# Kernel optimization log

Measured on AMD Instinct MI355X. Metric: run time of the kernel, lower is better.

## Reference

```python
import jax, jax.numpy as jnp
import numpy as np


def setup_inputs() -> dict:
    key = jax.random.key(0)
    ks = jax.random.split(key, 5)
    B, S, D = 2, 2048, 1024
    inv = 1.0 / np.sqrt(D)
    inp = {
        "x": jax.random.normal(ks[0], (B, S, D), jnp.float32),
        "Wq": jax.random.normal(ks[1], (D, D), jnp.float32) * inv,
        "bq": jnp.zeros((D,), jnp.float32),
        "Wk": jax.random.normal(ks[2], (D, D), jnp.float32) * inv,
        "bk": jnp.zeros((D,), jnp.float32),
        "Wv": jax.random.normal(ks[3], (D, D), jnp.float32) * inv,
        "bv": jnp.zeros((D,), jnp.float32),
        "Wo": jax.random.normal(ks[4], (D, D), jnp.float32) * inv,
        "bo": jnp.zeros((D,), jnp.float32),
        "num_heads": 16,
        "window_size": 128,
    }
    return inp


def reference(x, Wq, bq, Wk, bk, Wv, bv, Wo, bo, num_heads, window_size):
    B, S, D = x.shape
    H = num_heads
    hd = D // H
    scale = 1.0 / np.sqrt(hd)

    def split_heads(t):  # [B,S,D] -> [B,H,S,hd]
        return t.reshape(B, S, H, hd).transpose(0, 2, 1, 3)

    q = split_heads(x @ Wq + bq)
    k = split_heads(x @ Wk + bk)
    v = split_heads(x @ Wv + bv)

    # dense scores, then sliding-window + causal mask (faithful to original)
    scores = jnp.einsum('bhqd,bhkd->bhqk', q, k) * scale  # [B,H,S,S]
    i = jnp.arange(S)[:, None]
    j = jnp.arange(S)[None, :]
    # position i attends to j in [i - window_size + 1, i]
    mask = (j <= i) & (j > i - window_size)
    scores = jnp.where(mask, scores, -jnp.inf)
    attn_weights = jax.nn.softmax(scores, axis=-1)  # dropout is identity in eval

    out = jnp.einsum('bhqk,bhkd->bhqd', attn_weights, v)  # [B,H,S,hd]
    out = out.transpose(0, 2, 1, 3).reshape(B, S, D)
    return out @ Wo + bo, attn_weights
```

## Files before the change

### kernel.cpp

```cpp
#include <hip/hip_runtime.h>
#include <cmath>

typedef __attribute__((ext_vector_type(8))) __bf16 v8bf;
typedef __attribute__((ext_vector_type(4))) float  v4f;

#define DEV static __device__ __forceinline__

DEV unsigned short f2bf(float f) {
  unsigned u = __builtin_bit_cast(unsigned, f);
  unsigned r = u + 0x7fffu + ((u >> 16) & 1u);
  return (unsigned short)(r >> 16);
}
DEV float bf2f(unsigned short s) {
  return __builtin_bit_cast(float, ((unsigned)s) << 16);
}
DEV v8bf ld8(const unsigned short* p) { return *(const v8bf*)p; }

DEV void gl16(const unsigned short* g, unsigned short* l) {
  __builtin_amdgcn_global_load_lds(
      (const __attribute__((address_space(1))) unsigned int*)g,
      (__attribute__((address_space(3))) unsigned int*)l, 16, 0, 0);
}

DEV void zero_rows(float* __restrict__ wout, int rbase, int wave, int lane) {
  int r0 = rbase + wave * 4;
  for (int rr = 0; rr < 4; rr++) {
    int row = r0 + rr;
    int i = row & 2047;
    int lo = i - 127;
    float* rowp = wout + (size_t)row * 2048;
#pragma unroll
    for (int it = 0; it < 8; it++) {
      int col = it * 256 + lane * 4;
      bool overlap = (col + 3 >= lo) && (col <= i);
      if (!overlap) {
        v4f z = {0.f, 0.f, 0.f, 0.f};
        __builtin_nontemporal_store(z, (v4f*)(rowp + col));
      } else {
#pragma unroll
        for (int e = 0; e < 4; e++) {
          int j = col + e;
          if (j < lo || j > i) rowp[j] = 0.f;
        }
      }
    }
  }
}

__global__ __launch_bounds__(256) void k_prep(const float* __restrict__ x,
                                              const float* __restrict__ Wq,
                                              const float* __restrict__ Wk,
                                              const float* __restrict__ Wv,
                                              const float* __restrict__ Wo,
                                              const float* __restrict__ bq,
                                              const float* __restrict__ bk,
                                              const float* __restrict__ bv,
                                              unsigned short* __restrict__ xb,
                                              unsigned short* __restrict__ WT,
                                              unsigned short* __restrict__ WoT,
                                              float* __restrict__ bqkv) {
  __shared__ float t[32][33];
  int bx = blockIdx.x, tid = threadIdx.x;
  if (bx < 4096) {
    int i = bx * 256 + tid;
    float4 v = ((const float4*)x)[i];
    unsigned lo = (unsigned)f2bf(v.x) | ((unsigned)f2bf(v.y) << 16);
    unsigned hi = (unsigned)f2bf(v.z) | ((unsigned)f2bf(v.w) << 16);
    ((uint2*)xb)[i] = make_uint2(lo, hi);
  } else if (bx < 8192) {
    int rem = bx - 4096;
    int z = rem >> 10, r2 = rem & 1023;
    const float* src = (z == 0) ? Wq : (z == 1) ? Wk : (z == 2) ? Wv : Wo;
    unsigned short* dst = (z < 3) ? WT + z * 1048576 : WoT;
    int n0 = (r2 & 31) * 32, k0 = (r2 >> 5) * 32;
    int tx = tid & 31, ty = tid >> 5;
    for (int r = ty; r < 32; r += 8)
      t[r][tx] = src[(k0 + r) * 1024 + n0 + tx];
    __syncthreads();
    for (int r = ty; r < 32; r += 8)
      dst[(n0 + r) * 1024 + k0 + tx] = f2bf(t[tx][r]);
  } else {
    int i = (bx - 8192) * 256 + tid;
    float v = (i < 1024) ? bq[i] : (i < 2048 ? bk[i - 1024] : bv[i - 2048]);
    bqkv[i] = v;
  }
}

__global__ __launch_bounds__(256) void k_gemm1(const unsigned short* __restrict__ A,
                                               const unsigned short* __restrict__ Bt,
                                               const float* __restrict__ bias,
                                               unsigned short* __restrict__ QK,
                                               unsigned short* __restrict__ Vtg) {
  constexpr int K = 1024;
  __shared__ __attribute__((aligned(16))) unsigned short As[128 * 32];
  __shared__ __attribute__((aligned(16))) unsigned short Bs[128 * 32];
  int tid = threadIdx.x;
  int wave = tid >> 6, lane = tid & 63;
  int gid = blockIdx.x;
  int n0 = (gid % 24) * 128, m0 = (gid / 24) * 128;
  int wm = (wave >> 1) * 64, wn = (wave & 1) * 64;
  int m = lane & 15, q4 = lane >> 4;
  int arow = tid >> 2, acol = (tid & 3) * 8;
  v4f acc[4][4] = {};
  const unsigned short* ga0 = A + (m0 + arow) * K + acol;
  const unsigned short* ga1 = A + (m0 + 64 + arow) * K + acol;
  const unsigned short* gb0 = Bt + (n0 + arow) * K + acol;
  const unsigned short* gb1 = Bt + (n0 + 64 + arow) * K + acol;
  unsigned short* lA0 = As + wave * 512;
  unsigned short* lA1 = As + 2048 + wave * 512;
  unsigned short* lB0 = Bs + wave * 512;
  unsigned short* lB1 = Bs + 2048 + wave * 512;

  for (int kt = 0; kt < K; kt += 32) {
    gl16(ga0 + kt, lA0);
    gl16(ga1 + kt, lA1);
    gl16(gb0 + kt, lB0);
    gl16(gb1 + kt, lB1);
    __syncthreads();
    v8bf af[4], bfv[4];
#pragma unroll
    for (int mt = 0; mt < 4; mt++) af[mt] = ld8(&As[(wm + mt * 16 + m) * 32 + q4 * 8]);
#pragma unroll
    for (int nt = 0; nt < 4; nt++) bfv[nt] = ld8(&Bs[(wn + nt * 16 + m) * 32 + q4 * 8]);
#pragma unroll
    for (int mt = 0; mt < 4; mt++)
#pragma unroll
      for (int nt = 0; nt < 4; nt++)
        acc[mt][nt] = __builtin_amdgcn_mfma_f32_16x16x32_bf16(af[mt], bfv[nt], acc[mt][nt], 0, 0, 0);
    __syncthreads();
  }
  if (n0 < 2048) {
#pragma unroll
    for (int mt = 0; mt < 4; mt++)
#pragma unroll
      for (int nt = 0; nt < 4; nt++) {
        int col = n0 + wn + nt * 16 + m;
        float bb = bias[col];
#pragma unroll
        for (int r = 0; r < 4; r++) {
          int row = m0 + wm + mt * 16 + q4 * 4 + r;
          QK[row * 2048 + col] = f2bf(acc[mt][nt][r] + bb);
        }
      }
  } else {
    int b = m0 >> 11;
#pragma unroll
    for (int mt = 0; mt < 4; mt++)
#pragma unroll
      for (int nt = 0; nt < 4; nt++) {
        int d = n0 - 2048 + wn + nt * 16 + m;
        int h = d >> 6, dd = d & 63;
        float bb = bias[2048 + d];
        int vrow = (b * 16 + h) * 64 + dd;
        int s0 = (m0 + wm + mt * 16 + q4 * 4) & 2047;
        unsigned short u0 = f2bf(acc[mt][nt][0] + bb);
        unsigned short u1 = f2bf(acc[mt][nt][1] + bb);
        unsigned short u2 = f2bf(acc[mt][nt][2] + bb);
        unsigned short u3 = f2bf(acc[mt][nt][3] + bb);
        unsigned lo = (unsigned)u0 | ((unsigned)u1 << 16);
        unsigned hi = (unsigned)u2 | ((unsigned)u3 << 16);
        *(uint2*)&Vtg[(size_t)vrow * 2048 + s0] = make_uint2(lo, hi);
      }
  }
}

__global__ __launch_bounds__(256) void k_attn(const unsigned short* __restrict__ QK,
                                              const unsigned short* __restrict__ Vtg,
                                              unsigned short* __restrict__ Oatt,
                                              float* __restrict__ wout) {
  constexpr int VTS = 208;
  constexpr int PSS = 168;
  __shared__ __attribute__((aligned(16))) unsigned short Vt[64 * VTS];
  __shared__ __attribute__((aligned(16))) unsigned short Ps[4][16 * PSS];
  int tid = threadIdx.x, wave = tid >> 6, lane = tid & 63;
  int b = blockIdx.z, h = blockIdx.y, i0 = blockIdx.x * 64;
  int kbase = i0 - 128;
  const int ld = 2048;
  const unsigned short* Qg = QK + (size_t)b * 2048 * ld + h * 64;
  const unsigned short* Kg = Qg + 1024;

  const unsigned short* vsrc = Vtg + (size_t)(b * 16 + h) * 64 * 2048;
  for (int idx = tid; idx < 1536; idx += 256) {
    int row = idx / 24, c16 = idx % 24;
    int gcol = kbase + c16 * 8;
    if (gcol < 0) gcol = 0;
    v8bf vv = ld8(vsrc + (size_t)row * 2048 + gcol);
    *(v8bf*)&Vt[row * VTS + c16 * 8] = vv;
  }
  {
    int row = tid >> 2, c4 = (tid & 3) * 4;
    *(uint2*)&Vt[row * VTS + 192 + c4] = make_uint2(0u, 0u);
  }
  for (int c = lane; c < 16 * 24; c += 64)
    Ps[wave][(c / 24) * PSS + 144 + (c % 24)] = 0;
  __syncthreads();

  int qb = i0 + wave * 16;
  int m = lane & 15, q4 = lane >> 4;

  const unsigned short* qrow = Qg + (qb + m) * ld;
  v8bf qa0 = ld8(qrow + q4 * 8);
  v8bf qa1 = ld8(qrow + 32 + q4 * 8);

  v4f sc[9];
#pragma unroll
  for (int n = 0; n < 9; n++) {
    int key = kbase + wave * 16 + n * 16 + m;
    int kg = key < 0 ? 0 : key;
    const unsigned short* krow = Kg + kg * ld;
    v8bf kb0 = ld8(krow + q4 * 8);
    v8bf kb1 = ld8(krow + 32 + q4 * 8);
    v4f z = {0.f, 0.f, 0.f, 0.f};
    z = __builtin_amdgcn_mfma_f32_16x16x32_bf16(qa0, kb0, z, 0, 0, 0);
    z = __builtin_amdgcn_mfma_f32_16x16x32_bf16(qa1, kb1, z, 0, 0, 0);
    sc[n] = z;
  }
  float mx[4] = {-3e38f, -3e38f, -3e38f, -3e38f};
#pragma unroll
  for (int n = 0; n < 9; n++)
#pragma unroll
    for (int r = 0; r < 4; r++) {
      int i = qb + q4 * 4 + r;
      int j = kbase + wave * 16 + n * 16 + m;
      float v = sc[n][r] * 0.125f;
      bool ok = (j >= 0) && (j <= i) && (j > i - 128);
      v = ok ? v : -3e38f;
      sc[n][r] = v;
      mx[r] = fmaxf(mx[r], v);
    }
#pragma unroll
  for (int o = 1; o < 16; o <<= 1)
#pragma unroll
    for (int r = 0; r < 4; r++) mx[r] = fmaxf(mx[r], __shfl_xor(mx[r], o, 64));
  float sum[4] = {0.f, 0.f, 0.f, 0.f};
#pragma unroll
  for (int n = 0; n < 9; n++)
#pragma unroll
    for (int r = 0; r < 4; r++) {
      float p = __expf(sc[n][r] - mx[r]);
      sc[n][r] = p;
      sum[r] += p;
    }
#pragma unroll
  for (int o = 1; o < 16; o <<= 1)
#pragma unroll
    for (int r = 0; r < 4; r++) sum[r] += __shfl_xor(sum[r], o, 64);
  float inv[4];
#pragma unroll
  for (int r = 0; r < 4; r++) inv[r] = 1.0f / sum[r];

#pragma unroll
  for (int n = 0; n < 9; n++)
#pragma unroll
    for (int r = 0; r < 4; r++)
      Ps[wave][(q4 * 4 + r) * PSS + n * 16 + m] = f2bf(sc[n][r] * inv[r]);
  __syncthreads();

  v4f oacc[4] = {};
#pragma unroll
  for (int c = 0; c < 5; c++) {
    v8bf pa = ld8(&Ps[wave][m * PSS + c * 32 + q4 * 8]);
#pragma unroll
    for (int dt = 0; dt < 4; dt++) {
      v8bf vb = ld8(&Vt[(dt * 16 + m) * VTS + wave * 16 + c * 32 + q4 * 8]);
      oacc[dt] = __builtin_amdgcn_mfma_f32_16x16x32_bf16(pa, vb, oacc[dt], 0, 0, 0);
    }
  }
#pragma unroll
  for (int dt = 0; dt < 4; dt++)
#pragma unroll
    for (int r = 0; r < 4; r++)
      Oatt[(b * 2048 + qb + q4 * 4 + r) * 1024 + h * 64 + dt * 16 + m] = f2bf(oacc[dt][r]);

  for (int R = 0; R < 16; R++) {
    int iq = qb + R;
    float* rowp = wout + (size_t)((b * 16 + h) * 2048 + iq) * 2048;
    int lo = iq - 127;
    int t0 = R + 1 + lane * 2;
    float p0 = bf2f(Ps[wave][R * PSS + t0]);
    float p1 = bf2f(Ps[wave][R * PSS + t0 + 1]);
    int j0 = lo + lane * 2;
    if (j0 >= 0) rowp[j0] = p0;
    if (j0 + 1 >= 0) rowp[j0 + 1] = p1;
  }
}

__global__ __launch_bounds__(256) void k_tail(const unsigned short* __restrict__ Oat,
                                              const unsigned short* __restrict__ WoT,
                                              const float* __restrict__ bo,
                                              float* __restrict__ out,
                                              float* __restrict__ wout) {
  __shared__ __attribute__((aligned(16))) unsigned short As[128 * 32];
  __shared__ __attribute__((aligned(16))) unsigned short Bs[128 * 32];
  int tid = threadIdx.x, wave = tid >> 6, lane = tid & 63;
  int bx = blockIdx.x;

  if (bx >= 256) {
    zero_rows(wout, (bx - 256) * 16, wave, lane);
    return;
  }
  constexpr int K = 1024;
  int n0 = (bx & 7) * 128, m0 = (bx >> 3) * 128;
  int wm = (wave >> 1) * 64, wn = (wave & 1) * 64;
  int m = lane & 15, q4 = lane >> 4;
  int arow = tid >> 2, acol = (tid & 3) * 8;
  v4f acc[4][4] = {};
  const unsigned short* ga0 = Oat + (m0 + arow) * K + acol;
  const unsigned short* ga1 = Oat + (m0 + 64 + arow) * K + acol;
  const unsigned short* gb0 = WoT + (n0 + arow) * K + acol;
  const unsigned short* gb1 = WoT + (n0 + 64 + arow) * K + acol;
  unsigned short* lA0 = As + wave * 512;
  unsigned short* lA1 = As + 2048 + wave * 512;
  unsigned short* lB0 = Bs + wave * 512;
  unsigned short* lB1 = Bs + 2048 + wave * 512;
  for (int kt = 0; kt < K; kt += 32) {
    gl16(ga0 + kt, lA0);
    gl16(ga1 + kt, lA1);
    gl16(gb0 + kt, lB0);
    gl16(gb1 + kt, lB1);
    __syncthreads();
    v8bf af[4], bfv[4];
#pragma unroll
    for (int mt = 0; mt < 4; mt++) af[mt] = ld8(&As[(wm + mt * 16 + m) * 32 + q4 * 8]);
#pragma unroll
    for (int nt = 0; nt < 4; nt++) bfv[nt] = ld8(&Bs[(wn + nt * 16 + m) * 32 + q4 * 8]);
#pragma unroll
    for (int mt = 0; mt < 4; mt++)
#pragma unroll
      for (int nt = 0; nt < 4; nt++)
        acc[mt][nt] = __builtin_amdgcn_mfma_f32_16x16x32_bf16(af[mt], bfv[nt], acc[mt][nt], 0, 0, 0);
    __syncthreads();
  }
#pragma unroll
  for (int mt = 0; mt < 4; mt++)
#pragma unroll
    for (int nt = 0; nt < 4; nt++) {
      int col = n0 + wn + nt * 16 + m;
      float bb = bo[col];
#pragma unroll
      for (int r = 0; r < 4; r++) {
        int row = m0 + wm + mt * 16 + q4 * 4 + r;
        out[row * 1024 + col] = acc[mt][nt][r] + bb;
      }
    }
}

extern "C" void kernel_launch(void* const* d_in, const int* in_sizes, int n_in,
                              void* d_out, int out_size, void* d_ws, size_t ws_size,
                              hipStream_t stream) {
  (void)in_sizes; (void)n_in; (void)out_size; (void)ws_size;
  const float* x  = (const float*)d_in[0];
  const float* Wq = (const float*)d_in[1];
  const float* bq = (const float*)d_in[2];
  const float* Wk = (const float*)d_in[3];
  const float* bk = (const float*)d_in[4];
  const float* Wv = (const float*)d_in[5];
  const float* bv = (const float*)d_in[6];
  const float* Wo = (const float*)d_in[7];
  const float* bo = (const float*)d_in[8];

  char* ws = (char*)d_ws;
  unsigned short* xb   = (unsigned short*)(ws);
  unsigned short* WT   = (unsigned short*)(ws + 8388608);
  unsigned short* WoT  = (unsigned short*)(ws + 14680064);
  float*          bqkv = (float*)(ws + 16777216);
  unsigned short* QK   = (unsigned short*)(ws + 16789504);
  unsigned short* Oat  = (unsigned short*)(ws + 33566720);
  unsigned short* Vtg  = (unsigned short*)(ws + 41955328);

  float* out  = (float*)d_out;
  float* wout = out + 4194304;

  k_prep<<<8204, 256, 0, stream>>>(x, Wq, Wk, Wv, Wo, bq, bk, bv, xb, WT, WoT, bqkv);
  k_gemm1<<<768, 256, 0, stream>>>(xb, WT, bqkv, QK, Vtg);
  k_attn<<<dim3(32, 16, 2), 256, 0, stream>>>(QK, Vtg, Oat, wout);
  k_tail<<<4352, 256, 0, stream>>>(Oat, WoT, bo, out, wout);
}
```

Measured before the change: 657.8 us.

## Stage compact band weights and write full attention rows in one streaming pass

The attention kernel now writes each row's 128 banded probabilities as packed bf16 into a compact workspace buffer instead of scattering them into the dense fp32 weight matrix. The tail kernel's zeroing blocks then write every full row once with nontemporal vector stores, filling band entries from that buffer. The old split of masked partial zero writes plus separate scattered band writes is gone. The attention kernel also drops its LDS staging of V and reads V fragments directly from global memory, removing a block barrier at the cost of uncoalesced global loads.

```diff
diff --git a/kernel.cpp b/kernel.cpp
--- a/kernel.cpp
+++ b/kernel.cpp
@@ -20,31 +20,6 @@
   __builtin_amdgcn_global_load_lds(
       (const __attribute__((address_space(1))) unsigned int*)g,
       (__attribute__((address_space(3))) unsigned int*)l, 16, 0, 0);
-}
-
-DEV void zero_rows(float* __restrict__ wout, int rbase, int wave, int lane) {
-  int r0 = rbase + wave * 4;
-  for (int rr = 0; rr < 4; rr++) {
-    int row = r0 + rr;
-    int i = row & 2047;
-    int lo = i - 127;
-    float* rowp = wout + (size_t)row * 2048;
-#pragma unroll
-    for (int it = 0; it < 8; it++) {
-      int col = it * 256 + lane * 4;
-      bool overlap = (col + 3 >= lo) && (col <= i);
-      if (!overlap) {
-        v4f z = {0.f, 0.f, 0.f, 0.f};
-        __builtin_nontemporal_store(z, (v4f*)(rowp + col));
-      } else {
-#pragma unroll
-        for (int e = 0; e < 4; e++) {
-          int j = col + e;
-          if (j < lo || j > i) rowp[j] = 0.f;
-        }
-      }
-    }
-  }
 }
 
 __global__ __launch_bounds__(256) void k_prep(const float* __restrict__ x,
@@ -167,10 +142,8 @@
 __global__ __launch_bounds__(256) void k_attn(const unsigned short* __restrict__ QK,
                                               const unsigned short* __restrict__ Vtg,
                                               unsigned short* __restrict__ Oatt,
-                                              float* __restrict__ wout) {
-  constexpr int VTS = 208;
+                                              unsigned short* __restrict__ cb) {
   constexpr int PSS = 168;
-  __shared__ __attribute__((aligned(16))) unsigned short Vt[64 * VTS];
   __shared__ __attribute__((aligned(16))) unsigned short Ps[4][16 * PSS];
   int tid = threadIdx.x, wave = tid >> 6, lane = tid & 63;
   int b = blockIdx.z, h = blockIdx.y, i0 = blockIdx.x * 64;
@@ -178,22 +151,10 @@
   const int ld = 2048;
   const unsigned short* Qg = QK + (size_t)b * 2048 * ld + h * 64;
   const unsigned short* Kg = Qg + 1024;
-
   const unsigned short* vsrc = Vtg + (size_t)(b * 16 + h) * 64 * 2048;
-  for (int idx = tid; idx < 1536; idx += 256) {
-    int row = idx / 24, c16 = idx % 24;
-    int gcol = kbase + c16 * 8;
-    if (gcol < 0) gcol = 0;
-    v8bf vv = ld8(vsrc + (size_t)row * 2048 + gcol);
-    *(v8bf*)&Vt[row * VTS + c16 * 8] = vv;
-  }
-  {
-    int row = tid >> 2, c4 = (tid & 3) * 4;
-    *(uint2*)&Vt[row * VTS + 192 + c4] = make_uint2(0u, 0u);
-  }
+
   for (int c = lane; c < 16 * 24; c += 64)
     Ps[wave][(c / 24) * PSS + 144 + (c % 24)] = 0;
-  __syncthreads();
 
   int qb = i0 + wave * 16;
   int m = lane & 15, q4 = lane >> 4;
@@ -260,9 +221,12 @@
 #pragma unroll
   for (int c = 0; c < 5; c++) {
     v8bf pa = ld8(&Ps[wave][m * PSS + c * 32 + q4 * 8]);
+    int jc = kbase + wave * 16 + c * 32 + q4 * 8;
+    if (jc < 0) jc = 0;
+    if (jc > 2040) jc = 2040;
 #pragma unroll
     for (int dt = 0; dt < 4; dt++) {
-      v8bf vb = ld8(&Vt[(dt * 16 + m) * VTS + wave * 16 + c * 32 + q4 * 8]);
+      v8bf vb = ld8(vsrc + (size_t)(dt * 16 + m) * 2048 + jc);
       oacc[dt] = __builtin_amdgcn_mfma_f32_16x16x32_bf16(pa, vb, oacc[dt], 0, 0, 0);
     }
   }
@@ -273,15 +237,10 @@
       Oatt[(b * 2048 + qb + q4 * 4 + r) * 1024 + h * 64 + dt * 16 + m] = f2bf(oacc[dt][r]);
 
   for (int R = 0; R < 16; R++) {
-    int iq = qb + R;
-    float* rowp = wout + (size_t)((b * 16 + h) * 2048 + iq) * 2048;
-    int lo = iq - 127;
-    int t0 = R + 1 + lane * 2;
-    float p0 = bf2f(Ps[wave][R * PSS + t0]);
-    float p1 = bf2f(Ps[wave][R * PSS + t0 + 1]);
-    int j0 = lo + lane * 2;
-    if (j0 >= 0) rowp[j0] = p0;
-    if (j0 + 1 >= 0) rowp[j0 + 1] = p1;
+    int row = (b * 16 + h) * 2048 + qb + R;
+    unsigned short p0 = Ps[wave][R * PSS + R + 1 + lane * 2];
+    unsigned short p1 = Ps[wave][R * PSS + R + 2 + lane * 2];
+    ((unsigned*)cb)[row * 64 + lane] = (unsigned)p0 | ((unsigned)p1 << 16);
   }
 }
 
@@ -289,60 +248,83 @@
                                               const unsigned short* __restrict__ WoT,
                                               const float* __restrict__ bo,
                                               float* __restrict__ out,
+                                              const unsigned short* __restrict__ cb,
                                               float* __restrict__ wout) {
   __shared__ __attribute__((aligned(16))) unsigned short As[128 * 32];
   __shared__ __attribute__((aligned(16))) unsigned short Bs[128 * 32];
   int tid = threadIdx.x, wave = tid >> 6, lane = tid & 63;
-  int bx = blockIdx.x;
-
-  if (bx >= 256) {
-    zero_rows(wout, (bx - 256) * 16, wave, lane);
-    return;
-  }
-  constexpr int K = 1024;
-  int n0 = (bx & 7) * 128, m0 = (bx >> 3) * 128;
-  int wm = (wave >> 1) * 64, wn = (wave & 1) * 64;
-  int m = lane & 15, q4 = lane >> 4;
-  int arow = tid >> 2, acol = (tid & 3) * 8;
-  v4f acc[4][4] = {};
-  const unsigned short* ga0 = Oat + (m0 + arow) * K + acol;
-  const unsigned short* ga1 = Oat + (m0 + 64 + arow) * K + acol;
-  const unsigned short* gb0 = WoT + (n0 + arow) * K + acol;
-  const unsigned short* gb1 = WoT + (n0 + 64 + arow) * K + acol;
-  unsigned short* lA0 = As + wave * 512;
-  unsigned short* lA1 = As + 2048 + wave * 512;
-  unsigned short* lB0 = Bs + wave * 512;
-  unsigned short* lB1 = Bs + 2048 + wave * 512;
-  for (int kt = 0; kt < K; kt += 32) {
-    gl16(ga0 + kt, lA0);
-    gl16(ga1 + kt, lA1);
-    gl16(gb0 + kt, lB0);
-    gl16(gb1 + kt, lB1);
-    __syncthreads();
-    v8bf af[4], bfv[4];
-#pragma unroll
-    for (int mt = 0; mt < 4; mt++) af[mt] = ld8(&As[(wm + mt * 16 + m) * 32 + q4 * 8]);
-#pragma unroll
-    for (int nt = 0; nt < 4; nt++) bfv[nt] = ld8(&Bs[(wn + nt * 16 + m) * 32 + q4 * 8]);
+
+  if (blockIdx.x < 256) {
+    constexpr int K = 1024;
+    int bx = blockIdx.x;
+    int n0 = (bx & 7) * 128, m0 = (bx >> 3) * 128;
+    int wm = (wave >> 1) * 64, wn = (wave & 1) * 64;
+    int m = lane & 15, q4 = lane >> 4;
+    int arow = tid >> 2, acol = (tid & 3) * 8;
+    v4f acc[4][4] = {};
+    const unsigned short* ga0 = Oat + (m0 + arow) * K + acol;
+    const unsigned short* ga1 = Oat + (m0 + 64 + arow) * K + acol;
+    const unsigned short* gb0 = WoT + (n0 + arow) * K + acol;
+    const unsigned short* gb1 = WoT + (n0 + 64 + arow) * K + acol;
+    unsigned short* lA0 = As + wave * 512;
+    unsigned short* lA1 = As + 2048 + wave * 512;
+    unsigned short* lB0 = Bs + wave * 512;
+    unsigned short* lB1 = Bs + 2048 + wave * 512;
+    for (int kt = 0; kt < K; kt += 32) {
+      gl16(ga0 + kt, lA0);
+      gl16(ga1 + kt, lA1);
+      gl16(gb0 + kt, lB0);
+      gl16(gb1 + kt, lB1);
+      __syncthreads();
+      v8bf af[4], bfv[4];
+#pragma unroll
+      for (int mt = 0; mt < 4; mt++) af[mt] = ld8(&As[(wm + mt * 16 + m) * 32 + q4 * 8]);
+#pragma unroll
+      for (int nt = 0; nt < 4; nt++) bfv[nt] = ld8(&Bs[(wn + nt * 16 + m) * 32 + q4 * 8]);
+#pragma unroll
+      for (int mt = 0; mt < 4; mt++)
+#pragma unroll
+        for (int nt = 0; nt < 4; nt++)
+          acc[mt][nt] = __builtin_amdgcn_mfma_f32_16x16x32_bf16(af[mt], bfv[nt], acc[mt][nt], 0, 0, 0);
+      __syncthreads();
+    }
 #pragma unroll
     for (int mt = 0; mt < 4; mt++)
 #pragma unroll
-      for (int nt = 0; nt < 4; nt++)
-        acc[mt][nt] = __builtin_amdgcn_mfma_f32_16x16x32_bf16(af[mt], bfv[nt], acc[mt][nt], 0, 0, 0);
-    __syncthreads();
-  }
-#pragma unroll
-  for (int mt = 0; mt < 4; mt++)
-#pragma unroll
-    for (int nt = 0; nt < 4; nt++) {
-      int col = n0 + wn + nt * 16 + m;
-      float bb = bo[col];
-#pragma unroll
-      for (int r = 0; r < 4; r++) {
-        int row = m0 + wm + mt * 16 + q4 * 4 + r;
-        out[row * 1024 + col] = acc[mt][nt][r] + bb;
+      for (int nt = 0; nt < 4; nt++) {
+        int col = n0 + wn + nt * 16 + m;
+        float bb = bo[col];
+#pragma unroll
+        for (int r = 0; r < 4; r++) {
+          int row = m0 + wm + mt * 16 + q4 * 4 + r;
+          out[row * 1024 + col] = acc[mt][nt][r] + bb;
+        }
       }
-    }
+  } else {
+    int wb = blockIdx.x - 256;
+    int rbase = wb * 16 + wave * 4;
+    for (int rr = 0; rr < 4; rr++) {
+      int row = rbase + rr;
+      int i = row & 2047;
+      float* rowp = wout + (size_t)row * 2048;
+      const unsigned short* crow = cb + (size_t)row * 128;
+      int lo = i - 127;
+#pragma unroll
+      for (int it = 0; it < 8; it++) {
+        int col = it * 256 + lane * 4;
+        v4f v = {0.f, 0.f, 0.f, 0.f};
+        if (col <= i && col + 3 >= lo) {
+#pragma unroll
+          for (int e = 0; e < 4; e++) {
+            int j = col + e;
+            if (j >= lo && j <= i && j >= 0)
+              v[e] = bf2f(crow[j - lo]);
+          }
+        }
+        __builtin_nontemporal_store(v, (v4f*)(rowp + col));
+      }
+    }
+  }
 }
 
 extern "C" void kernel_launch(void* const* d_in, const int* in_sizes, int n_in,
@@ -367,12 +349,13 @@
   unsigned short* QK   = (unsigned short*)(ws + 16789504);
   unsigned short* Oat  = (unsigned short*)(ws + 33566720);
   unsigned short* Vtg  = (unsigned short*)(ws + 41955328);
+  unsigned short* cb   = (unsigned short*)(ws + 50343936);
 
   float* out  = (float*)d_out;
   float* wout = out + 4194304;
 
   k_prep<<<8204, 256, 0, stream>>>(x, Wq, Wk, Wv, Wo, bq, bk, bv, xb, WT, WoT, bqkv);
   k_gemm1<<<768, 256, 0, stream>>>(xb, WT, bqkv, QK, Vtg);
-  k_attn<<<dim3(32, 16, 2), 256, 0, stream>>>(QK, Vtg, Oat, wout);
-  k_tail<<<4352, 256, 0, stream>>>(Oat, WoT, bo, out, wout);
-}
+  k_attn<<<dim3(32, 16, 2), 256, 0, stream>>>(QK, Vtg, Oat, cb);
+  k_tail<<<4352, 256, 0, stream>>>(Oat, WoT, bo, out, cb, wout);
+}
```

Measured after the change: 650.1 us. About the same (-1.2%).
